# Kernel tuning notes

Hardware: AMD Instinct MI355X
Metric: run time of the kernel (lower is better)

The kernel has to match this reference:

```python
import jax, jax.numpy as jnp
import numpy as np

D_MODEL = 1024
NUM_HEADS = 16
DEPTH = D_MODEL // NUM_HEADS


def setup_inputs() -> dict:
    key = jax.random.key(0)
    ks = jax.random.split(key, 8)
    B, S, D = 2, 2048, D_MODEL
    s = 1.0 / np.sqrt(D)
    return {
        "q": jax.random.normal(ks[0], (B, S, D), jnp.float32),
        "k": jax.random.normal(ks[1], (B, S, D), jnp.float32),
        "v": jax.random.normal(ks[2], (B, S, D), jnp.float32),
        "Wq": jax.random.normal(ks[3], (D, D), jnp.float32) * s,
        "bq": jnp.zeros((D,), jnp.float32),
        "Wk": jax.random.normal(ks[4], (D, D), jnp.float32) * s,
        "bk": jnp.zeros((D,), jnp.float32),
        "Wv": jax.random.normal(ks[5], (D, D), jnp.float32) * s,
        "bv": jnp.zeros((D,), jnp.float32),
        "Wo": jax.random.normal(ks[6], (D, D), jnp.float32) * s,
        "bo": jnp.zeros((D,), jnp.float32),
    }


def _split_heads(x):
    # [B,S,D] -> [B,H,S,depth]
    B, S, _ = x.shape
    return x.reshape(B, S, NUM_HEADS, DEPTH).transpose(0, 2, 1, 3)


def reference(q, k, v, Wq, bq, Wk, bk, Wv, bv, Wo, bo):
    qh = _split_heads(q @ Wq + bq)  # [B,H,S,d]
    kh = _split_heads(k @ Wk + bk)
    vh = _split_heads(v @ Wv + bv)
    scale = 1.0 / jnp.sqrt(jnp.float32(DEPTH))
    logits = jnp.einsum("bhqd,bhkd->bhqk", qh, kh) * scale  # [B,H,S,S]
    weights = jax.nn.softmax(logits, axis=-1)
    attn = jnp.einsum("bhqk,bhkd->bhqd", weights, vh)
    B, H, S, d = attn.shape
    attn = attn.transpose(0, 2, 1, 3).reshape(B, S, H * d)  # [B,S,D]
    return attn @ Wo + bo
```

## Files before the change

### kernel.cpp

```cpp
#include <hip/hip_runtime.h>
#include <hip/hip_bf16.h>
#include <stdint.h>


typedef __attribute__((ext_vector_type(8))) short bf16x8;
typedef __attribute__((ext_vector_type(4))) float f32x4;

#define MFMA16(a, b, c) __builtin_amdgcn_mfma_f32_16x16x32_bf16((a), (b), (c), 0, 0, 0)
#define EXP2(x) __builtin_amdgcn_exp2f(x)

static constexpr int S_LEN = 2048;
static constexpr int DM    = 1024;
static constexpr int DEPTH = 64;
static constexpr float QSCALE = 0.125f * 1.44269504088896340736f;

__device__ __forceinline__ unsigned short f2b(float f) {
  unsigned u = __float_as_uint(f);
  unsigned r = 0x7FFFu + ((u >> 16) & 1u);
  return (unsigned short)((u + r) >> 16);
}

__device__ __forceinline__ unsigned short b16(float f) {
  __hip_bfloat16 h = __float2bfloat16(f);
  union { __hip_bfloat16 h; unsigned short u; } c; c.h = h; return c.u;
}

__device__ __forceinline__ void gload16(const void* g, void* l) {
  __builtin_amdgcn_global_load_lds(
      (const __attribute__((address_space(1))) void*)g,
      (__attribute__((address_space(3))) void*)l, 16, 0, 0);
}

__device__ __forceinline__ void wave_lds_fence() {
  asm volatile("" ::: "memory");
  __builtin_amdgcn_sched_barrier(0);
}

__global__ __launch_bounds__(256) void prep_k(
    const float* __restrict__ xq, const float* __restrict__ xk,
    const float* __restrict__ xv, unsigned short* __restrict__ Xb,
    const float* __restrict__ Wq, const float* __restrict__ Wk,
    const float* __restrict__ Wv, const float* __restrict__ Wo,
    unsigned short* __restrict__ Wt) {
  __shared__ unsigned short ts[64][68];
  const int bid = blockIdx.x;
  const int tid = threadIdx.x;
  if (bid < 6144) {
    const int which = bid >> 11;
    const int xb = bid & 2047;
    const float* X = (which == 0) ? xq : (which == 1) ? xk : xv;
    size_t gid = ((size_t)xb * 256 + tid) * 8;
    float4 v0 = *(const float4*)&X[gid];
    float4 v1 = *(const float4*)&X[gid + 4];
    union { unsigned short u[8]; bf16x8 v; } pk;
    pk.u[0] = f2b(v0.x); pk.u[1] = f2b(v0.y); pk.u[2] = f2b(v0.z); pk.u[3] = f2b(v0.w);
    pk.u[4] = f2b(v1.x); pk.u[5] = f2b(v1.y); pk.u[6] = f2b(v1.z); pk.u[7] = f2b(v1.w);
    *(bf16x8*)&Xb[(size_t)which * 4096 * DM + gid] = pk.v;
    return;
  }
  const int wb = bid - 6144;
  const int w = wb >> 8, tile = wb & 255;
  const int tr = tile >> 4, tc = tile & 15;
  const float* W = (w == 0) ? Wq : (w == 1) ? Wk : (w == 2) ? Wv : Wo;
  unsigned short* T = Wt + (size_t)w * DM * DM;
  const int kr = tid >> 4, nc = (tid & 15) * 4;
  #pragma unroll
  for (int j = 0; j < 4; ++j) {
    int k = tr * 64 + kr + j * 16;
    float4 v = *(const float4*)&W[(size_t)k * DM + tc * 64 + nc];
    ushort4 u; u.x = f2b(v.x); u.y = f2b(v.y); u.z = f2b(v.z); u.w = f2b(v.w);
    *(ushort4*)&ts[kr + j * 16][nc] = u;
  }
  __syncthreads();
  const int nr = tid >> 4, kc = (tid & 15) * 4;
  #pragma unroll
  for (int j = 0; j < 4; ++j) {
    int n = tc * 64 + nr + j * 16;
    ushort4 u;
    u.x = ts[kc + 0][nr + j * 16];
    u.y = ts[kc + 1][nr + j * 16];
    u.z = ts[kc + 2][nr + j * 16];
    u.w = ts[kc + 3][nr + j * 16];
    *(ushort4*)&T[(size_t)n * DM + tr * 64 + kc] = u;
  }
}

__global__ __launch_bounds__(256, 4) void proj_qkv_k(
    const unsigned short* __restrict__ Xb, const unsigned short* __restrict__ Wt,
    const float* __restrict__ bq, const float* __restrict__ bk, const float* __restrict__ bv,
    unsigned short* __restrict__ Qh, unsigned short* __restrict__ Kh,
    unsigned short* __restrict__ Vt) {
  __shared__ __align__(16) unsigned short As[2][128][32];
  __shared__ __align__(16) unsigned short Bs[2][128][32];

  const int z = blockIdx.z;
  const unsigned short* A  = Xb + (size_t)z * 4096 * DM;
  const unsigned short* Bt = Wt + (size_t)z * DM * DM;
  const float* bias = (z == 0) ? bq : (z == 1) ? bk : bv;
  const float scale = (z == 0) ? QSCALE : 1.0f;
  unsigned short* O = (z == 0) ? Qh : (z == 1) ? Kh : Vt;

  const int bm = blockIdx.x, bn = blockIdx.y;
  const int tid = threadIdx.x;
  const int wave = tid >> 6, lane = tid & 63;
  const int wr = wave >> 1, wc = wave & 1;
  const int g = lane >> 4, i16 = lane & 15;
  const int srow = tid >> 2, sslot = tid & 3;

  f32x4 acc[4][4] = {};

  auto stage = [&](int ks, int buf) {
    #pragma unroll
    for (int rnd = 0; rnd < 2; ++rnd) {
      int row = rnd * 64 + srow;
      int sw = sslot ^ ((row >> 1) & 3);
      gload16(&A[(size_t)(bm * 128 + row) * DM + ks * 32 + sw * 8],
              &As[buf][row][sslot * 8]);
      gload16(&Bt[(size_t)(bn * 128 + row) * DM + ks * 32 + sw * 8],
              &Bs[buf][row][sslot * 8]);
    }
  };
  auto compute = [&](int buf) {
    bf16x8 a[4], b[4];
    #pragma unroll
    for (int m = 0; m < 4; ++m) {
      int row = wr * 64 + m * 16 + i16;
      int sl = g ^ ((row >> 1) & 3);
      a[m] = *(const bf16x8*)&As[buf][row][sl * 8];
    }
    #pragma unroll
    for (int n = 0; n < 4; ++n) {
      int row = wc * 64 + n * 16 + i16;
      int sl = g ^ ((row >> 1) & 3);
      b[n] = *(const bf16x8*)&Bs[buf][row][sl * 8];
    }
    #pragma unroll
    for (int m = 0; m < 4; ++m)
      #pragma unroll
      for (int n = 0; n < 4; ++n)
        acc[m][n] = MFMA16(a[m], b[n], acc[m][n]);
  };

  stage(0, 0);
  __syncthreads();
  int cur = 0;
  #pragma unroll 1
  for (int ks = 0; ks < DM / 32; ++ks) {
    if (ks + 1 < DM / 32) stage(ks + 1, cur ^ 1);
    compute(cur);
    __syncthreads();
    cur ^= 1;
  }

  #pragma unroll
  for (int m = 0; m < 4; ++m) {
    #pragma unroll
    for (int n = 0; n < 4; ++n) {
      #pragma unroll
      for (int r = 0; r < 4; ++r) {
        int row = bm * 128 + wr * 64 + m * 16 + g * 4 + r;
        int col = bn * 128 + wc * 64 + n * 16 + i16;
        float v = (acc[m][n][r] + bias[col]) * scale;
        int b_ = row >> 11, s = row & 2047;
        int h = col >> 6, dd = col & 63;
        if (z != 2)
          O[(((size_t)(b_ * 16 + h)) * S_LEN + s) * DEPTH + dd] = f2b(v);
        else
          O[(((size_t)(b_ * 16 + h)) * DEPTH + dd) * S_LEN + s] = f2b(v);
      }
    }
  }
}

__global__ __launch_bounds__(256, 4) void out_proj_k(
    const unsigned short* __restrict__ At, const unsigned short* __restrict__ Wto,
    const float* __restrict__ bo, float* __restrict__ out) {
  __shared__ __align__(16) unsigned short As[2][64][32];
  __shared__ __align__(16) unsigned short Bs[2][128][32];

  const int bm = blockIdx.x, bn = blockIdx.y;
  const int tid = threadIdx.x;
  const int wave = tid >> 6, lane = tid & 63;
  const int wr = wave >> 1, wc = wave & 1;
  const int g = lane >> 4, i16 = lane & 15;
  const int srow = tid >> 2, sslot = tid & 3;

  f32x4 acc[2][4] = {};

  auto stage = [&](int ks, int buf) {
    {
      int sw = sslot ^ ((srow >> 1) & 3);
      gload16(&At[(size_t)(bm * 64 + srow) * DM + ks * 32 + sw * 8],
              &As[buf][srow][sslot * 8]);
    }
    #pragma unroll
    for (int rnd = 0; rnd < 2; ++rnd) {
      int row = rnd * 64 + srow;
      int sw = sslot ^ ((row >> 1) & 3);
      gload16(&Wto[(size_t)(bn * 128 + row) * DM + ks * 32 + sw * 8],
              &Bs[buf][row][sslot * 8]);
    }
  };
  auto compute = [&](int buf) {
    bf16x8 a[2], b[4];
    #pragma unroll
    for (int m = 0; m < 2; ++m) {
      int row = wr * 32 + m * 16 + i16;
      int sl = g ^ ((row >> 1) & 3);
      a[m] = *(const bf16x8*)&As[buf][row][sl * 8];
    }
    #pragma unroll
    for (int n = 0; n < 4; ++n) {
      int row = wc * 64 + n * 16 + i16;
      int sl = g ^ ((row >> 1) & 3);
      b[n] = *(const bf16x8*)&Bs[buf][row][sl * 8];
    }
    #pragma unroll
    for (int m = 0; m < 2; ++m)
      #pragma unroll
      for (int n = 0; n < 4; ++n)
        acc[m][n] = MFMA16(a[m], b[n], acc[m][n]);
  };

  stage(0, 0);
  __syncthreads();
  int cur = 0;
  #pragma unroll 1
  for (int ks = 0; ks < DM / 32; ++ks) {
    if (ks + 1 < DM / 32) stage(ks + 1, cur ^ 1);
    compute(cur);
    __syncthreads();
    cur ^= 1;
  }

  #pragma unroll
  for (int m = 0; m < 2; ++m) {
    #pragma unroll
    for (int n = 0; n < 4; ++n) {
      #pragma unroll
      for (int r = 0; r < 4; ++r) {
        int row = bm * 64 + wr * 32 + m * 16 + g * 4 + r;
        int col = bn * 128 + wc * 64 + n * 16 + i16;
        out[(size_t)row * DM + col] = acc[m][n][r] + bo[col];
      }
    }
  }
}

__global__ __launch_bounds__(256) void attn_k(
    const unsigned short* __restrict__ Qh, const unsigned short* __restrict__ Kh,
    const unsigned short* __restrict__ Vt, unsigned short* __restrict__ Ob) {
  __shared__ unsigned short kv_lds[2][2][64][64];
  __shared__ unsigned short p_lds[4][2][16][64];

  const int linear = blockIdx.y * 16 + blockIdx.x;
  const int wg = (linear & 7) * 64 + (linear >> 3);
  const int qt = wg & 15, bh = wg >> 4;

  const int tid = threadIdx.x;
  const int wave = tid >> 6, lane = tid & 63;
  const int g = lane >> 4, i16 = lane & 15;

  const unsigned short* Q = Qh + (size_t)bh * S_LEN * DEPTH;
  const unsigned short* K = Kh + (size_t)bh * S_LEN * DEPTH;
  const unsigned short* V = Vt + (size_t)bh * DEPTH * S_LEN;

  const int sr0 = tid >> 3;
  const int ss0 = tid & 7;

  const int qbase = qt * 128 + wave * 32;
  bf16x8 qa[2][2];
  #pragma unroll
  for (int qs = 0; qs < 2; ++qs) {
    qa[qs][0] = *(const bf16x8*)&Q[(size_t)(qbase + qs * 16 + i16) * DEPTH + g * 8];
    qa[qs][1] = *(const bf16x8*)&Q[(size_t)(qbase + qs * 16 + i16) * DEPTH + 32 + g * 8];
  }

  const short one_b = (short)0x3F80;
  const bf16x8 ones = {one_b, one_b, one_b, one_b, one_b, one_b, one_b, one_b};

  f32x4 l_acc[2] = {};
  f32x4 o[2][4] = {};

  #pragma unroll
  for (int j = 0; j < 2; ++j) {
    int r = j * 32 + sr0;
    int sw = ss0 ^ (r & 7);
    gload16(&K[(size_t)r * DEPTH + sw * 8], &kv_lds[0][0][r][ss0 * 8]);
    gload16(&V[(size_t)r * S_LEN + sw * 8], &kv_lds[0][1][r][ss0 * 8]);
  }
  __syncthreads();

  int cur = 0;
  #pragma unroll 1
  for (int t64 = 0; t64 < 32; ++t64) {
    const int kv0 = t64 * 64;
    if (t64 + 1 < 32) {
      const int nkv = kv0 + 64;
      #pragma unroll
      for (int j = 0; j < 2; ++j) {
        int r = j * 32 + sr0;
        int sw = ss0 ^ (r & 7);
        gload16(&K[(size_t)(nkv + r) * DEPTH + sw * 8], &kv_lds[cur ^ 1][0][r][ss0 * 8]);
        gload16(&V[(size_t)r * S_LEN + nkv + sw * 8],   &kv_lds[cur ^ 1][1][r][ss0 * 8]);
      }
    }

    f32x4 sT[2][4];
    const f32x4 zero = {0.f, 0.f, 0.f, 0.f};
    __builtin_amdgcn_s_setprio(1);
    #pragma unroll
    for (int t = 0; t < 4; ++t) {
      int row = t * 16 + i16;
      int x = row & 7;
      bf16x8 k0 = *(const bf16x8*)&kv_lds[cur][0][row][(g ^ x) * 8];
      bf16x8 k1 = *(const bf16x8*)&kv_lds[cur][0][row][((4 + g) ^ x) * 8];
      #pragma unroll
      for (int qs = 0; qs < 2; ++qs) {
        f32x4 s = MFMA16(k0, qa[qs][0], zero);
        sT[qs][t] = MFMA16(k1, qa[qs][1], s);
      }
    }
    __builtin_amdgcn_s_setprio(0);

    #pragma unroll
    for (int qs = 0; qs < 2; ++qs) {
      #pragma unroll
      for (int t = 0; t < 4; ++t) {
        ushort4 w;
        w.x = b16(EXP2(sT[qs][t][0]));
        w.y = b16(EXP2(sT[qs][t][1]));
        w.z = b16(EXP2(sT[qs][t][2]));
        w.w = b16(EXP2(sT[qs][t][3]));
        int idx = (((t * 2 + (g >> 1)) ^ (i16 & 7)) * 8) + (g & 1) * 4;
        *(ushort4*)&p_lds[wave][qs][i16][idx] = w;
      }
    }
    wave_lds_fence();
    bf16x8 pa0[2], pa1[2];
    #pragma unroll
    for (int qs = 0; qs < 2; ++qs) {
      pa0[qs] = *(const bf16x8*)&p_lds[wave][qs][i16][(g ^ (i16 & 7)) * 8];
      pa1[qs] = *(const bf16x8*)&p_lds[wave][qs][i16][((4 + g) ^ (i16 & 7)) * 8];
    }

    __builtin_amdgcn_s_setprio(1);
    #pragma unroll
    for (int dt = 0; dt < 4; ++dt) {
      int row = dt * 16 + i16;
      int x = row & 7;
      bf16x8 v0 = *(const bf16x8*)&kv_lds[cur][1][row][(g ^ x) * 8];
      bf16x8 v1 = *(const bf16x8*)&kv_lds[cur][1][row][((4 + g) ^ x) * 8];
      #pragma unroll
      for (int qs = 0; qs < 2; ++qs) {
        o[qs][dt] = MFMA16(pa0[qs], v0, o[qs][dt]);
        o[qs][dt] = MFMA16(pa1[qs], v1, o[qs][dt]);
      }
    }
    #pragma unroll
    for (int qs = 0; qs < 2; ++qs) {
      l_acc[qs] = MFMA16(pa0[qs], ones, l_acc[qs]);
      l_acc[qs] = MFMA16(pa1[qs], ones, l_acc[qs]);
    }
    __builtin_amdgcn_s_setprio(0);

    __syncthreads();
    cur ^= 1;
  }

  const int b_ = bh >> 4, h = bh & 15;
  #pragma unroll
  for (int qs = 0; qs < 2; ++qs) {
    f32x4 rinv;
    #pragma unroll
    for (int r = 0; r < 4; ++r)
      rinv[r] = 1.0f / l_acc[qs][r];
    #pragma unroll
    for (int dt = 0; dt < 4; ++dt) {
      #pragma unroll
      for (int r = 0; r < 4; ++r) {
        int qrow = qbase + qs * 16 + g * 4 + r;
        float val = o[qs][dt][r] * rinv[r];
        Ob[((size_t)(b_ * S_LEN + qrow)) * DM + h * DEPTH + dt * 16 + i16] = f2b(val);
      }
    }
  }
}

extern "C" void kernel_launch(void* const* d_in, const int* in_sizes, int n_in,
                              void* d_out, int out_size, void* d_ws, size_t ws_size,
                              hipStream_t stream) {
  const float* q  = (const float*)d_in[0];
  const float* k  = (const float*)d_in[1];
  const float* v  = (const float*)d_in[2];
  const float* Wq = (const float*)d_in[3];
  const float* bq = (const float*)d_in[4];
  const float* Wk = (const float*)d_in[5];
  const float* bk = (const float*)d_in[6];
  const float* Wv = (const float*)d_in[7];
  const float* bv = (const float*)d_in[8];
  const float* Wo = (const float*)d_in[9];
  const float* bo = (const float*)d_in[10];
  float* out = (float*)d_out;

  const size_t HEAD_ELEMS = (size_t)2 * 16 * S_LEN * DEPTH;
  unsigned short* Qh = (unsigned short*)d_ws;
  unsigned short* Kh = Qh + HEAD_ELEMS;
  unsigned short* Vt = Kh + HEAD_ELEMS;
  unsigned short* Xb = Vt + HEAD_ELEMS;
  unsigned short* At = Xb;
  unsigned short* Wt = Xb + 3 * HEAD_ELEMS;

  dim3 blk(256);
  hipLaunchKernelGGL(prep_k, dim3(7168), blk, 0, stream,
                     q, k, v, Xb, Wq, Wk, Wv, Wo, Wt);
  hipLaunchKernelGGL(proj_qkv_k, dim3(32, 8, 3), blk, 0, stream,
                     Xb, Wt, bq, bk, bv, Qh, Kh, Vt);
  hipLaunchKernelGGL(attn_k, dim3(16, 32), blk, 0, stream, Qh, Kh, Vt, At);
  hipLaunchKernelGGL(out_proj_k, dim3(64, 8), blk, 0, stream,
                     At, Wt + (size_t)3 * DM * DM, bo, out);
}
```

Before: 124.5 us.

## Triple-buffer K/V tiles in attention with prefetch distance two

Moves the attention kernel's K/V LDS staging from double buffering to a three-buffer ring that prefetches two tiles ahead. Each iteration waits on a partial vmcnt count and a single barrier, replacing the full __syncthreads at the end of the loop body. The aim is to hide global-to-LDS load latency better and to drop one barrier per iteration. It costs 16KB more LDS per block, which may lower occupancy, and correctness depends on the hand-written vmcnt counts matching the number of outstanding loads.

```diff
diff --git a/kernel.cpp b/kernel.cpp
--- a/kernel.cpp
+++ b/kernel.cpp
@@ -250,7 +250,7 @@
 __global__ __launch_bounds__(256) void attn_k(
     const unsigned short* __restrict__ Qh, const unsigned short* __restrict__ Kh,
     const unsigned short* __restrict__ Vt, unsigned short* __restrict__ Ob) {
-  __shared__ unsigned short kv_lds[2][2][64][64];
+  __shared__ unsigned short kv_lds[3][2][64][64];
   __shared__ unsigned short p_lds[4][2][16][64];
 
   const int linear = blockIdx.y * 16 + blockIdx.x;
@@ -282,29 +282,28 @@
   f32x4 l_acc[2] = {};
   f32x4 o[2][4] = {};
 
-  #pragma unroll
-  for (int j = 0; j < 2; ++j) {
-    int r = j * 32 + sr0;
-    int sw = ss0 ^ (r & 7);
-    gload16(&K[(size_t)r * DEPTH + sw * 8], &kv_lds[0][0][r][ss0 * 8]);
-    gload16(&V[(size_t)r * S_LEN + sw * 8], &kv_lds[0][1][r][ss0 * 8]);
-  }
-  __syncthreads();
-
-  int cur = 0;
+  auto stage = [&](int t, int buf) {
+    const int kv = t * 64;
+    #pragma unroll
+    for (int j = 0; j < 2; ++j) {
+      int r = j * 32 + sr0;
+      int sw = ss0 ^ (r & 7);
+      gload16(&K[(size_t)(kv + r) * DEPTH + sw * 8], &kv_lds[buf][0][r][ss0 * 8]);
+      gload16(&V[(size_t)r * S_LEN + kv + sw * 8],   &kv_lds[buf][1][r][ss0 * 8]);
+    }
+  };
+
+  stage(0, 0);
+  stage(1, 1);
+  int b0 = 0, b1 = 1, b2 = 2;
+
   #pragma unroll 1
   for (int t64 = 0; t64 < 32; ++t64) {
-    const int kv0 = t64 * 64;
-    if (t64 + 1 < 32) {
-      const int nkv = kv0 + 64;
-      #pragma unroll
-      for (int j = 0; j < 2; ++j) {
-        int r = j * 32 + sr0;
-        int sw = ss0 ^ (r & 7);
-        gload16(&K[(size_t)(nkv + r) * DEPTH + sw * 8], &kv_lds[cur ^ 1][0][r][ss0 * 8]);
-        gload16(&V[(size_t)r * S_LEN + nkv + sw * 8],   &kv_lds[cur ^ 1][1][r][ss0 * 8]);
-      }
-    }
+    if (t64 < 30) { asm volatile("s_waitcnt vmcnt(4)" ::: "memory"); }
+    else          { asm volatile("s_waitcnt vmcnt(0)" ::: "memory"); }
+    __builtin_amdgcn_s_barrier();
+    asm volatile("" ::: "memory");
+    if (t64 + 2 < 32) stage(t64 + 2, b2);
 
     f32x4 sT[2][4];
     const f32x4 zero = {0.f, 0.f, 0.f, 0.f};
@@ -313,8 +312,8 @@
     for (int t = 0; t < 4; ++t) {
       int row = t * 16 + i16;
       int x = row & 7;
-      bf16x8 k0 = *(const bf16x8*)&kv_lds[cur][0][row][(g ^ x) * 8];
-      bf16x8 k1 = *(const bf16x8*)&kv_lds[cur][0][row][((4 + g) ^ x) * 8];
+      bf16x8 k0 = *(const bf16x8*)&kv_lds[b0][0][row][(g ^ x) * 8];
+      bf16x8 k1 = *(const bf16x8*)&kv_lds[b0][0][row][((4 + g) ^ x) * 8];
       #pragma unroll
       for (int qs = 0; qs < 2; ++qs) {
         f32x4 s = MFMA16(k0, qa[qs][0], zero);
@@ -349,8 +348,8 @@
     for (int dt = 0; dt < 4; ++dt) {
       int row = dt * 16 + i16;
       int x = row & 7;
-      bf16x8 v0 = *(const bf16x8*)&kv_lds[cur][1][row][(g ^ x) * 8];
-      bf16x8 v1 = *(const bf16x8*)&kv_lds[cur][1][row][((4 + g) ^ x) * 8];
+      bf16x8 v0 = *(const bf16x8*)&kv_lds[b0][1][row][(g ^ x) * 8];
+      bf16x8 v1 = *(const bf16x8*)&kv_lds[b0][1][row][((4 + g) ^ x) * 8];
       #pragma unroll
       for (int qs = 0; qs < 2; ++qs) {
         o[qs][dt] = MFMA16(pa0[qs], v0, o[qs][dt]);
@@ -364,8 +363,7 @@
     }
     __builtin_amdgcn_s_setprio(0);
 
-    __syncthreads();
-    cur ^= 1;
+    int tmp = b0; b0 = b1; b1 = b2; b2 = tmp;
   }
 
   const int b_ = bh >> 4, h = bh & 15;
```

Result: no change. 125.1 us (+0.5%).
